# Kernel optimization log

Hardware: AMD Instinct MI355X
Metric: run time of the kernel (lower is better)

Reference implementation:

```python
import jax, jax.numpy as jnp
import numpy as np


def _build_ring_index(H):
    """Precompute static (row, col) source-index maps for the square
    rotational unrolling. Output maps have shape [ceil(H/2), 4*H].

    For ring i (from center outward, dif = lmid - i), each output row is the
    concatenation of 9 segments exactly matching the torch slice/repeat/flip
    sequence, totalling 4H-4 columns, then the first 4 columns are copied to
    the last 4 (the tail wrap in the original code).
    """
    W = H
    lmid = (H - 1) // 2
    Hr = (H + 1) // 2
    rows = np.zeros((Hr, 4 * H), dtype=np.int32)
    cols = np.zeros((Hr, 4 * H), dtype=np.int32)
    for i in range(lmid, -1, -1):
        dif = lmid - i
        el = 2 * dif if H % 2 == 1 else 2 * dif + 1
        r, c = [], []
        # corner (i,i) repeated i times
        r += [i] * i;                    c += [i] * i
        # top edge, left-to-right
        r += [i] * el;                   c += list(range(i, i + el))
        # top-right corner repeated 2i
        r += [i] * (2 * i);              c += [W - i - 1] * (2 * i)
        # right edge, top-to-bottom
        r += list(range(i, i + el));     c += [W - i - 1] * el
        # bottom-right corner repeated 2i
        r += [i + el] * (2 * i);         c += [i + el] * (2 * i)
        # bottom edge, right-to-left (fliplr of img[i+el, i+1:i+1+el])
        r += [i + el] * el;              c += list(range(i + el, i, -1))
        # bottom-left corner repeated 2i
        r += [i + el] * (2 * i);         c += [i] * (2 * i)
        # left edge, bottom-to-top (fliplr of img[i+1:i+1+el, i])
        r += list(range(i + el, i, -1)); c += [i] * el
        # corner (i,i) repeated i times
        r += [i] * i;                    c += [i] * i
        # total length is always 4H-4; wrap first 4 entries to the tail
        r += r[:4];                      c += c[:4]
        rows[dif] = r
        cols[dif] = c
    return rows, cols


def setup_inputs() -> dict:
    key = jax.random.key(0)
    x = jax.random.normal(key, (16, 32, 512, 512), dtype=jnp.float32)
    return {"x": x}


def reference(x) -> jnp.ndarray:
    B, C, H, W = x.shape
    rows, cols = _build_ring_index(H)  # static, shape [ceil(H/2), 4H]
    # single fused gather replacing the ring-wise python loop
    return x[:, :, jnp.asarray(rows), jnp.asarray(cols)]
```

## Files before the change

### kernel.cpp

```cpp
#include <hip/hip_runtime.h>


#define SQRL_H 512
#define SQRL_IMG ((size_t)SQRL_H * SQRL_H)
#define SQRL_ROWW 2048
#define SQRL_NR 256

__global__ __launch_bounds__(256) void sqrl_gather_kernel(
    const float* __restrict__ x, float4* __restrict__ out, long n4) {
    long t = (long)blockIdx.x * blockDim.x + threadIdx.x;
    if (t >= n4) return;

    int  j4  = (int)(t & 511);
    long row = t >> 9;
    int  dif = (int)(row & 255);
    long img = row >> 8;

    const float* __restrict__ base = x + img * SQRL_IMG;

    const int i_ = 255 - dif;
    const int el = 2 * dif + 1;
    const int b1 = i_ + el;
    const int b2 = b1 + 2 * i_;
    const int b3 = b2 + el;
    const int b4 = b3 + 2 * i_;
    const int b5 = b4 + el;
    const int b6 = b5 + 2 * i_;
    const int b7 = b6 + el;

    const int j0 = j4 * 4;
    float4 v;
    float* vp = reinterpret_cast<float*>(&v);
#pragma unroll
    for (int k = 0; k < 4; ++k) {
        int j  = j0 + k;
        int jj = (j >= 2044) ? (j - 2044) : j;
        int r, c;
        if (jj < b1)      { r = i_;       c = (jj > i_) ? jj : i_; }
        else if (jj < b3) { c = 511 - i_; int d = jj - b2; r = i_ + (d > 0 ? d : 0); }
        else if (jj < b5) { r = b1;       int d = jj - b4; c = b1 - (d > 0 ? d : 0); }
        else if (jj < b7) { c = i_;       int d = jj - b6; r = b1 - (d > 0 ? d : 0); }
        else              { r = i_;       c = i_; }
        vp[k] = base[(size_t)r * SQRL_H + c];
    }
    out[t] = v;
}

extern "C" void kernel_launch(void* const* d_in, const int* in_sizes, int n_in,
                              void* d_out, int out_size, void* d_ws, size_t ws_size,
                              hipStream_t stream) {
    const float* x = (const float*)d_in[0];
    float4* out = (float4*)d_out;
    long n4 = (long)out_size / 4;
    long nblocks = (n4 + 255) / 256;
    sqrl_gather_kernel<<<dim3((unsigned)nblocks), dim3(256), 0, stream>>>(x, out, n4);
}
```

Before: 1.717 ms.

## Transpose vertical ring edges through LDS tiles for coalesced gather

The vertical-edge segments (right and left ring edges) previously gathered column-strided input, one uncoalesced element per lane. A new set of blocks loads 64x64 input tiles row-wise into shared memory and writes the vertical-edge outputs transposed, so both reads and writes are coalesced. The original per-element path skips those segments and falls back to masked scalar stores for partial vectors. This adds extra blocks, LDS traffic, and split store paths.

```diff
diff --git a/kernel.cpp b/kernel.cpp
--- a/kernel.cpp
+++ b/kernel.cpp
@@ -4,18 +4,90 @@
 #define SQRL_H 512
 #define SQRL_IMG ((size_t)SQRL_H * SQRL_H)
 #define SQRL_ROWW 2048
-#define SQRL_NR 256
+#define NB_PER_IMG 72
 
-__global__ __launch_bounds__(256) void sqrl_gather_kernel(
-    const float* __restrict__ x, float4* __restrict__ out, long n4) {
-    long t = (long)blockIdx.x * blockDim.x + threadIdx.x;
-    if (t >= n4) return;
+__global__ __launch_bounds__(256) void sqrl_kernel(
+    const float* __restrict__ x, float* __restrict__ outf, long n4, long nB) {
+    __shared__ float lds[64][65];
+    const long bid = blockIdx.x;
 
-    int  j4  = (int)(t & 511);
-    long row = t >> 9;
-    int  dif = (int)(row & 255);
-    long img = row >> 8;
+    if (bid < nB) {
+        const int  rem  = (int)(bid % NB_PER_IMG);
+        const long img  = bid / NB_PER_IMG;
+        const int  jt   = rem % 9;
+        const int  dt   = (rem / 9) & 3;
+        const int  side = rem / 36;
+        const int  dif0 = dt * 64;
+        const int  j0   = (side == 0 ? 448 : 1472) + 64 * jt;
+        const int  ctr  = (side == 0) ? 766 : 1788;
 
+        int jmin;
+        if (j0 <= ctr && ctr < j0 + 64) jmin = 0;
+        else {
+            int a = j0 - ctr;        if (a < 0) a = -a;
+            int b = j0 + 63 - ctr;   if (b < 0) b = -b;
+            jmin = a < b ? a : b;
+        }
+        const int dmax = dif0 + 63;
+        if (dmax < jmin) return;
+
+        const int rlo = (side == 0) ? (j0 - 511) : (1981 - j0);
+        const int clo = (side == 0) ? (256 + dif0) : (192 - dif0);
+        const int rc  = (side == 0) ? 255 : 256;
+        const float* __restrict__ base = x + img * SQRL_IMG;
+        const int t = (int)threadIdx.x;
+
+        {
+            const int lr = t >> 2;
+            const int q  = t & 3;
+            const int r  = rlo + lr;
+            if ((unsigned)r < 512u) {
+                int adr = r - rc; if (adr < 0) adr = -adr;
+                if (adr <= dmax) {
+                    const float* rowp = base + (size_t)r * SQRL_H;
+#pragma unroll
+                    for (int k = 0; k < 4; ++k) {
+                        const int c0 = (q + 4 * k) * 4;
+                        const bool need = (side == 0)
+                            ? (clo + c0 + 3 >= 256 + adr)
+                            : (clo + c0     <= 255 - adr);
+                        if (need) {
+                            const float4 v = *reinterpret_cast<const float4*>(rowp + clo + c0);
+                            lds[lr][c0 + 0] = v.x;
+                            lds[lr][c0 + 1] = v.y;
+                            lds[lr][c0 + 2] = v.z;
+                            lds[lr][c0 + 3] = v.w;
+                        }
+                    }
+                }
+            }
+        }
+        __syncthreads();
+
+        const int jl   = t & 63;
+        const int dgrp = t >> 6;
+        const int j    = j0 + jl;
+        int adj = j - ctr; if (adj < 0) adj = -adj;
+        const int lj = (side == 0) ? jl : (63 - jl);
+        float* const orow = outf + ((size_t)img * 256 + dif0) * SQRL_ROWW + j;
+#pragma unroll
+        for (int it = 0; it < 16; ++it) {
+            const int dl = dgrp + 4 * it;
+            if (dif0 + dl >= adj) {
+                const int lc = (side == 0) ? dl : (63 - dl);
+                orow[(size_t)dl * SQRL_ROWW] = lds[lj][lc];
+            }
+        }
+        return;
+    }
+
+    const long tA = (bid - nB) * 256 + threadIdx.x;
+    if (tA >= n4) return;
+
+    const int  j4  = (int)(tA & 511);
+    const long row = tA >> 9;
+    const int  dif = (int)(row & 255);
+    const long img = row >> 8;
     const float* __restrict__ base = x + img * SQRL_IMG;
 
     const int i_ = 255 - dif;
@@ -31,10 +103,13 @@
     const int j0 = j4 * 4;
     float4 v;
     float* vp = reinterpret_cast<float*>(&v);
+    unsigned vm = 0;
 #pragma unroll
     for (int k = 0; k < 4; ++k) {
-        int j  = j0 + k;
-        int jj = (j >= 2044) ? (j - 2044) : j;
+        const int j  = j0 + k;
+        const int jj = (j >= 2044) ? (j - 2044) : j;
+        const bool vert = (jj >= b2 && jj < b3) || (jj >= b6 && jj < b7);
+        if (vert) { vm |= 1u << k; vp[k] = 0.0f; continue; }
         int r, c;
         if (jj < b1)      { r = i_;       c = (jj > i_) ? jj : i_; }
         else if (jj < b3) { c = 511 - i_; int d = jj - b2; r = i_ + (d > 0 ? d : 0); }
@@ -43,15 +118,24 @@
         else              { r = i_;       c = i_; }
         vp[k] = base[(size_t)r * SQRL_H + c];
     }
-    out[t] = v;
+    if (vm == 0u) {
+        *reinterpret_cast<float4*>(outf + (size_t)tA * 4) = v;
+    } else if (vm != 15u) {
+#pragma unroll
+        for (int k = 0; k < 4; ++k)
+            if (!(vm & (1u << k))) outf[(size_t)tA * 4 + k] = vp[k];
+    }
 }
 
 extern "C" void kernel_launch(void* const* d_in, const int* in_sizes, int n_in,
                               void* d_out, int out_size, void* d_ws, size_t ws_size,
                               hipStream_t stream) {
     const float* x = (const float*)d_in[0];
-    float4* out = (float4*)d_out;
-    long n4 = (long)out_size / 4;
-    long nblocks = (n4 + 255) / 256;
-    sqrl_gather_kernel<<<dim3((unsigned)nblocks), dim3(256), 0, stream>>>(x, out, n4);
+    float* outf = (float*)d_out;
+    long n4   = (long)out_size / 4;
+    long nA   = (n4 + 255) / 256;
+    long nimg = n4 >> 17;
+    long nB   = nimg * NB_PER_IMG;
+    long nblocks = nA + nB;
+    sqrl_kernel<<<dim3((unsigned)nblocks), dim3(256), 0, stream>>>(x, outf, n4, nB);
 }
```

Result: no change. 1.714 ms (-0.2%).
